# Optimization experiments

Hardware: AMD Instinct MI355X
Metric: run time of the kernel (lower is better)

Reference implementation:

```python
import jax, jax.numpy as jnp
import numpy as np

B, S, V, E, H, T = 128, 512, 6000, 100, 256, 9


def setup_inputs() -> dict:
    key = jax.random.key(0)
    ks = jax.random.split(key, 16)
    lengths = jax.random.randint(ks[0], (B,), S // 4, S + 1)
    mask = (jnp.arange(S)[None, :] < lengths[:, None])  # [B,S] bool, contiguous prefixes
    data = jax.random.randint(ks[1], (B, S), 1, V)
    data = jnp.where(mask, data, 0)  # pad token = 0 (padding_idx)
    sc = 0.1
    emb = jax.random.normal(ks[2], (V, E), jnp.float32) * sc
    emb = emb.at[0].set(0.0)  # padding_idx=0
    return {
        "data": data, "mask": mask,
        "emb": emb,
        "W_ih_f": jax.random.normal(ks[3], (4 * H, E), jnp.float32) * sc,
        "W_hh_f": jax.random.normal(ks[4], (4 * H, H), jnp.float32) * sc,
        "b_f": jax.random.normal(ks[5], (4 * H,), jnp.float32) * sc,
        "W_ih_b": jax.random.normal(ks[6], (4 * H, E), jnp.float32) * sc,
        "W_hh_b": jax.random.normal(ks[7], (4 * H, H), jnp.float32) * sc,
        "b_b": jax.random.normal(ks[8], (4 * H,), jnp.float32) * sc,
        "mlp_W": jax.random.normal(ks[9], (T, 2 * H), jnp.float32) * sc,
        "mlp_b": jax.random.normal(ks[10], (T,), jnp.float32) * sc,
        "start_trans": jax.random.normal(ks[11], (T,), jnp.float32) * sc,
        "trans": jax.random.normal(ks[12], (T, T), jnp.float32) * sc,
        "end_trans": jax.random.normal(ks[13], (T,), jnp.float32) * sc,
    }


def _lstm_dir(xg, W_hh, reverse):
    # xg: [S,B,4H] precomputed input projection + biases
    h0 = jnp.zeros((xg.shape[1], W_hh.shape[1]), xg.dtype)

    def step(carry, xt):
        h, c = carry
        g = xt + h @ W_hh.T
        i, f, gg, o = jnp.split(g, 4, axis=-1)  # PyTorch gate order i,f,g,o
        c = jax.nn.sigmoid(f) * c + jax.nn.sigmoid(i) * jnp.tanh(gg)
        h = jax.nn.sigmoid(o) * jnp.tanh(c)
        return (h, c), h

    _, hs = jax.lax.scan(step, (h0, h0), xg, reverse=reverse)
    return hs  # [S,B,H]


def _emissions(data, emb, W_ih_f, W_hh_f, b_f, W_ih_b, W_hh_b, b_b, mlp_W, mlp_b):
    x = emb[data]  # [B,S,E]
    xg_f = jnp.einsum('bse,ge->sbg', x, W_ih_f) + b_f
    xg_b = jnp.einsum('bse,ge->sbg', x, W_ih_b) + b_b
    hf = _lstm_dir(xg_f, W_hh_f, False)
    hb = _lstm_dir(xg_b, W_hh_b, True)
    h = jnp.concatenate([hf, hb], axis=-1)  # [S,B,2H]
    return jnp.einsum('sbh,th->bst', h, mlp_W) + mlp_b  # [B,S,T]


def _viterbi(em, mask, start_trans, trans, end_trans):
    b, s, t = em.shape
    score0 = start_trans + em[:, 0]  # [B,T]
    em_t = jnp.swapaxes(em, 0, 1)[1:]      # [S-1,B,T]
    mask_t = jnp.swapaxes(mask, 0, 1)[1:]  # [S-1,B]

    def step(score, inp):
        e_t, m_t = inp
        cand = score[:, :, None] + trans[None] + e_t[:, None, :]  # [B,Tprev,Tcur]
        new = cand.max(axis=1)
        bp = cand.argmax(axis=1).astype(jnp.int32)  # [B,T]
        score = jnp.where(m_t[:, None], new, score)
        return score, bp

    score, bps = jax.lax.scan(step, score0, (em_t, mask_t))
    final = score + end_trans
    best_score = final.max(axis=-1)               # [B]
    last_tag = final.argmax(axis=-1).astype(jnp.int32)

    def back(tag, inp):
        bp, m_t = inp
        prev = jnp.take_along_axis(bp, tag[:, None], axis=1)[:, 0]
        prev = jnp.where(m_t, prev, tag)
        return prev, tag

    first_tag, tags_rest = jax.lax.scan(back, last_tag, (bps, mask_t), reverse=True)
    paths = jnp.concatenate([first_tag[None], tags_rest], axis=0)  # [S,B]
    paths = jnp.where(jnp.swapaxes(mask, 0, 1), paths, 0)
    return jnp.swapaxes(paths, 0, 1), best_score


def reference(data, mask, emb, W_ih_f, W_hh_f, b_f, W_ih_b, W_hh_b, b_b,
              mlp_W, mlp_b, start_trans, trans, end_trans):
    em = _emissions(data, emb, W_ih_f, W_hh_f, b_f, W_ih_b, W_hh_b, b_b, mlp_W, mlp_b)
    paths, best_score = _viterbi(em, mask, start_trans, trans, end_trans)
    return paths, best_score
```

## Files before the change

### kernel.cpp

```cpp
#include <hip/hip_runtime.h>
#include <math.h>
#include <stdint.h>

#define B 128
#define S 512
#define V 6000
#define E 100
#define H 256
#define G4 1024
#define T 9

#define WREG 20
#define WLDS 3
#define WSTR 41

#define OFF_PEMB_F 0u
#define PEMB_BYTES (V*G4*4u)
#define OFF_PEMB_B (OFF_PEMB_F + PEMB_BYTES)
#define OFF_EMF    (OFF_PEMB_B + PEMB_BYTES)
#define EM_BYTES   (B*S*T*4u)
#define OFF_EMB    (OFF_EMF + EM_BYTES)
#define OFF_BP     (OFF_EMB + EM_BYTES)
#define BP_BYTES   ((S-1)*B*16u)
#define OFF_LT     (OFF_BP + BP_BYTES)
#define OFF_PT     (OFF_LT + 512u)
#define OFF_WSTREAM OFF_BP

__device__ __forceinline__ float sigf(float x) { return 1.0f / (1.0f + expf(-x)); }

__global__ __launch_bounds__(256) void k_pemb(const float* __restrict__ emb,
                                              const float* __restrict__ wf, const float* __restrict__ bf,
                                              const float* __restrict__ wb, const float* __restrict__ bb,
                                              char* __restrict__ ws) {
    int blk = blockIdx.x;
    int d   = blk >= 375;
    int vb  = d ? blk - 375 : blk;
    const float* W    = d ? wb : wf;
    const float* bias = d ? bb : bf;
    float* pe = (float*)(ws + (d ? OFF_PEMB_B : OFF_PEMB_F));

    __shared__ float es[16 * E];
    for (int i = threadIdx.x; i < 16 * E; i += 256) es[i] = emb[vb * 16 * E + i];
    __syncthreads();

    int j = threadIdx.x;
    float acc[4][16];
    #pragma unroll
    for (int q = 0; q < 4; q++) {
        float bq = bias[q * H + j];
        #pragma unroll
        for (int v = 0; v < 16; v++) acc[q][v] = bq;
    }
    for (int e = 0; e < E; e++) {
        float w0 = W[(0 * H + j) * E + e];
        float w1 = W[(1 * H + j) * E + e];
        float w2 = W[(2 * H + j) * E + e];
        float w3 = W[(3 * H + j) * E + e];
        #pragma unroll
        for (int v = 0; v < 16; v++) {
            float x = es[v * E + e];
            acc[0][v] += w0 * x; acc[1][v] += w1 * x;
            acc[2][v] += w2 * x; acc[3][v] += w3 * x;
        }
    }
    for (int v = 0; v < 16; v++)
        #pragma unroll
        for (int q = 0; q < 4; q++)
            pe[(vb * 16 + v) * G4 + q * H + j] = acc[q][v];
}

__global__ __launch_bounds__(256) void k_prep(const float* __restrict__ whhf,
                                              const float* __restrict__ whhb,
                                              char* __restrict__ ws) {
    int tid = blockIdx.x * 256 + threadIdx.x;
    if (tid >= 2 * WSTR * 1024) return;
    int d   = tid >= WSTR * 1024;
    int idx = d ? tid - WSTR * 1024 : tid;
    int g = idx >> 10, r = idx & 1023;
    const float* whh = d ? whhb : whhf;
    float4* wstr = (float4*)(ws + OFF_WSTREAM);
    const float4* src = (const float4*)(whh + (size_t)r * H + 4 * (WREG + WLDS));
    wstr[((size_t)(d * WSTR + g) << 10) + r] = src[g];
}

__global__ __attribute__((amdgpu_flat_work_group_size(512, 512), amdgpu_waves_per_eu(2, 2)))
void k_lstm(const int* __restrict__ data,
            const float* __restrict__ whhf,
            const float* __restrict__ whhb,
            const float* __restrict__ mlpW,
            char* __restrict__ ws) {
    int blk = blockIdx.x;
    int d = blk >> 7, b = blk & 127;
    const float* whh = d ? whhb : whhf;
    const float* pe  = (const float*)(ws + (d ? OFF_PEMB_B : OFF_PEMB_F));
    float* emdst = (float*)(ws + (d ? OFF_EMB : OFF_EMF));
    const float4* wstr = (const float4*)(ws + OFF_WSTREAM) + ((size_t)(d * WSTR) << 10);

    __shared__ __align__(16) float hs[H];
    __shared__ float4 sW[WLDS << 10];
    __shared__ float  gbuf[G4];
    __shared__ float  red[T][4];
    __shared__ int    toks[S];

    int t = threadIdx.x;
    int r0 = t, r1 = t + 512;

    const float4* wrow0 = (const float4*)(whh + (size_t)r0 * H);
    const float4* wrow1 = (const float4*)(whh + (size_t)r1 * H);
    float4 wA[WREG], wB[WREG];
    #pragma unroll
    for (int g = 0; g < WREG; g++) { wA[g] = wrow0[g]; wB[g] = wrow1[g]; }
    #pragma unroll
    for (int g = 0; g < WREG; g++) {
        asm volatile("" : "+v"(wA[g].x), "+v"(wA[g].y), "+v"(wA[g].z), "+v"(wA[g].w));
        asm volatile("" : "+v"(wB[g].x), "+v"(wB[g].y), "+v"(wB[g].z), "+v"(wB[g].w));
    }
    #pragma unroll
    for (int g = 0; g < WLDS; g++) {
        sW[(g << 10) + r0] = wrow0[WREG + g];
        sW[(g << 10) + r1] = wrow1[WREG + g];
    }

    toks[t] = data[b * S + t];

    float mw[T];
    if (t < 256) {
        #pragma unroll
        for (int tt = 0; tt < T; tt++) mw[tt] = mlpW[tt * (2 * H) + d * H + t];
    }
    if (t < H) hs[t] = 0.0f;
    float cst = 0.0f;
    __syncthreads();

    const float4* hs4 = (const float4*)hs;
    const float4* wsp0 = wstr + r0;
    const float4* wsp1 = wstr + r1;

    float pf0, pf1;
    {
        int sp0 = d ? (S - 1) : 0;
        size_t tok = (size_t)toks[sp0];
        pf0 = pe[(tok << 10) + r0];
        pf1 = pe[(tok << 10) + r1];
    }

    for (int ss = 0; ss < S; ss++) {
        int sp = d ? (S - 1 - ss) : ss;
        float acc0 = pf0, acc1 = pf1;
        if (ss + 1 < S) {
            int spn = d ? (S - 2 - ss) : (ss + 1);
            size_t tok = (size_t)toks[spn];
            pf0 = pe[(tok << 10) + r0];
            pf1 = pe[(tok << 10) + r1];
        }

        #pragma unroll
        for (int g = 0; g < WREG; g++) {
            float4 h4 = hs4[g];
            float4 a = wA[g], bb2 = wB[g];
            acc0 = fmaf(a.x, h4.x, acc0);  acc1 = fmaf(bb2.x, h4.x, acc1);
            acc0 = fmaf(a.y, h4.y, acc0);  acc1 = fmaf(bb2.y, h4.y, acc1);
            acc0 = fmaf(a.z, h4.z, acc0);  acc1 = fmaf(bb2.z, h4.z, acc1);
            acc0 = fmaf(a.w, h4.w, acc0);  acc1 = fmaf(bb2.w, h4.w, acc1);
        }
        #pragma unroll
        for (int g = 0; g < WLDS; g++) {
            float4 w0 = sW[(g << 10) + r0];
            float4 w1 = sW[(g << 10) + r1];
            float4 h4 = hs4[WREG + g];
            acc0 = fmaf(w0.x, h4.x, acc0);  acc1 = fmaf(w1.x, h4.x, acc1);
            acc0 = fmaf(w0.y, h4.y, acc0);  acc1 = fmaf(w1.y, h4.y, acc1);
            acc0 = fmaf(w0.z, h4.z, acc0);  acc1 = fmaf(w1.z, h4.z, acc1);
            acc0 = fmaf(w0.w, h4.w, acc0);  acc1 = fmaf(w1.w, h4.w, acc1);
        }
        #pragma unroll 4
        for (int g = 0; g < WSTR; g++) {
            float4 w0 = wsp0[(size_t)g << 10];
            float4 w1 = wsp1[(size_t)g << 10];
            float4 h4 = hs4[WREG + WLDS + g];
            acc0 = fmaf(w0.x, h4.x, acc0);  acc1 = fmaf(w1.x, h4.x, acc1);
            acc0 = fmaf(w0.y, h4.y, acc0);  acc1 = fmaf(w1.y, h4.y, acc1);
            acc0 = fmaf(w0.z, h4.z, acc0);  acc1 = fmaf(w1.z, h4.z, acc1);
            acc0 = fmaf(w0.w, h4.w, acc0);  acc1 = fmaf(w1.w, h4.w, acc1);
        }
        gbuf[r0] = acc0;
        gbuf[r1] = acc1;
        __syncthreads();

        if (t < 256) {
            float gi = gbuf[t], gf = gbuf[H + t], gg = gbuf[2 * H + t], go = gbuf[3 * H + t];
            float ig = sigf(gi), fg = sigf(gf), tg = tanhf(gg), og = sigf(go);
            cst = fg * cst + ig * tg;
            float hn = og * tanhf(cst);
            hs[t] = hn;
            int l = t & 63, wv = t >> 6;
            #pragma unroll
            for (int tt = 0; tt < T; tt++) {
                float v = hn * mw[tt];
                v += __shfl_xor(v, 32, 64); v += __shfl_xor(v, 16, 64);
                v += __shfl_xor(v, 8, 64);  v += __shfl_xor(v, 4, 64);
                v += __shfl_xor(v, 2, 64);  v += __shfl_xor(v, 1, 64);
                if (l == 0) red[tt][wv] = v;
            }
        }
        __syncthreads();
        if (t < T)
            emdst[((size_t)b * S + sp) * T + t] = red[t][0] + red[t][1] + red[t][2] + red[t][3];
    }
}

__global__ __launch_bounds__(64) void k_vit(const int* __restrict__ data,
                                            const float* __restrict__ strans,
                                            const float* __restrict__ trans,
                                            const float* __restrict__ etrans,
                                            const float* __restrict__ mlpb,
                                            float* __restrict__ out,
                                            char* __restrict__ ws) {
    int b = blockIdx.x, t = threadIdx.x;
    const float* emf = (const float*)(ws + OFF_EMF);
    const float* emb = (const float*)(ws + OFF_EMB);
    char* bp = ws + OFF_BP;
    int*  lt = (int*)(ws + OFF_LT);
    bool act = t < T;

    float trp[T];
    float mb = 0.0f;
    if (act) {
        #pragma unroll
        for (int p = 0; p < T; p++) trp[p] = trans[p * T + t];
        mb = mlpb[t];
    }
    float score = -1e30f;
    if (act) score = strans[t] + emf[(b * S) * T + t] + emb[(b * S) * T + t] + mb;

    for (int s = 1; s < S; s++) {
        float e = 0.0f;
        if (act) e = emf[(b * S + s) * T + t] + emb[(b * S + s) * T + t] + mb;
        float best = __shfl(score, 0, 64) + trp[0];
        int bpi = 0;
        #pragma unroll
        for (int p = 1; p < T; p++) {
            float cand = __shfl(score, p, 64) + trp[p];
            if (cand > best) { best = cand; bpi = p; }
        }
        int m = data[b * S + s] != 0;
        if (act) {
            score = m ? (best + e) : score;
            bp[((size_t)(s - 1) * B + b) * 16 + t] = (char)bpi;
        }
    }
    float fin = act ? score + etrans[t] : -1e30f;
    float bv = __shfl(fin, 0, 64);
    int bi = 0;
    #pragma unroll
    for (int p = 1; p < T; p++) {
        float v = __shfl(fin, p, 64);
        if (v > bv) { bv = v; bi = p; }
    }
    if (t == 0) { out[B * S + b] = bv; lt[b] = bi; }
}

__global__ __launch_bounds__(128) void k_back(const int* __restrict__ data, char* __restrict__ ws) {
    int b = threadIdx.x;
    const int4* bp4 = (const int4*)(ws + OFF_BP);
    const int*  lt  = (const int*)(ws + OFF_LT);
    int* pt = (int*)(ws + OFF_PT);
    int tag = lt[b];
    pt[(S - 1) * B + b] = tag;
    for (int p = S - 2; p >= 0; p--) {
        int4 r = bp4[(size_t)p * B + b];
        int m = data[b * S + p + 1] != 0;
        unsigned w = (unsigned)(tag < 8 ? (tag < 4 ? r.x : r.y) : r.z);
        int nt = (int)((w >> ((tag & 3) * 8)) & 0xff);
        tag = m ? nt : tag;
        pt[p * B + b] = tag;
    }
}

__global__ __launch_bounds__(256) void k_fin(const int* __restrict__ data,
                                             float* __restrict__ out,
                                             const char* __restrict__ ws) {
    int tid = blockIdx.x * 256 + threadIdx.x;
    const int* pt = (const int*)(ws + OFF_PT);
    int b = tid >> 9, p = tid & 511;
    out[tid] = (data[tid] != 0) ? (float)pt[p * B + b] : 0.0f;
}

extern "C" void kernel_launch(void* const* d_in, const int* in_sizes, int n_in,
                              void* d_out, int out_size, void* d_ws, size_t ws_size,
                              hipStream_t stream) {
    const int*   data = (const int*)d_in[0];
    const float* emb  = (const float*)d_in[2];
    const float* wihf = (const float*)d_in[3];
    const float* whhf = (const float*)d_in[4];
    const float* bf   = (const float*)d_in[5];
    const float* wihb = (const float*)d_in[6];
    const float* whhb = (const float*)d_in[7];
    const float* bb   = (const float*)d_in[8];
    const float* mlpW = (const float*)d_in[9];
    const float* mlpb = (const float*)d_in[10];
    const float* st   = (const float*)d_in[11];
    const float* tr   = (const float*)d_in[12];
    const float* et   = (const float*)d_in[13];
    float* out = (float*)d_out;
    char*  ws  = (char*)d_ws;

    hipLaunchKernelGGL(k_pemb, dim3(750),  dim3(256), 0, stream, emb, wihf, bf, wihb, bb, ws);
    hipLaunchKernelGGL(k_prep, dim3(328),  dim3(256), 0, stream, whhf, whhb, ws);
    hipLaunchKernelGGL(k_lstm, dim3(256),  dim3(512), 0, stream, data, whhf, whhb, mlpW, ws);
    hipLaunchKernelGGL(k_vit,  dim3(128),  dim3(64),  0, stream, data, st, tr, et, mlpb, out, ws);
    hipLaunchKernelGGL(k_back, dim3(1),    dim3(128), 0, stream, data, ws);
    hipLaunchKernelGGL(k_fin,  dim3(256),  dim3(256), 0, stream, data, out, ws);
}
```

Before: 4.772 ms.

## Process two batch rows per LSTM block with all four gates per thread

The recurrent LSTM kernel now handles two sequences per block with 256 threads, each computing all four gates of one hidden unit for both sequences. Each weight load is reused across two batch rows, and the gate-exchange shared buffer and one barrier per step are removed. h is double-buffered and the emission store is deferred by one step. The register-resident weight slice is dropped in favour of reading those columns from global/L2 each step, and the LDS weight share is increased. The trade-off is half as many blocks (128 instead of 256) and more global weight traffic per step.

```diff
diff --git a/kernel.cpp b/kernel.cpp
--- a/kernel.cpp
+++ b/kernel.cpp
@@ -10,8 +10,8 @@
 #define G4 1024
 #define T 9
 
-#define WREG 20
-#define WLDS 3
+#define WGLOB 15
+#define WLDS 8
 #define WSTR 41
 
 #define OFF_PEMB_F 0u
@@ -79,133 +79,209 @@
     int g = idx >> 10, r = idx & 1023;
     const float* whh = d ? whhb : whhf;
     float4* wstr = (float4*)(ws + OFF_WSTREAM);
-    const float4* src = (const float4*)(whh + (size_t)r * H + 4 * (WREG + WLDS));
+    const float4* src = (const float4*)(whh + (size_t)r * H + 4 * (WGLOB + WLDS));
     wstr[((size_t)(d * WSTR + g) << 10) + r] = src[g];
 }
 
-__global__ __attribute__((amdgpu_flat_work_group_size(512, 512), amdgpu_waves_per_eu(2, 2)))
+__global__ __attribute__((amdgpu_flat_work_group_size(256, 256), amdgpu_waves_per_eu(1, 1)))
 void k_lstm(const int* __restrict__ data,
             const float* __restrict__ whhf,
             const float* __restrict__ whhb,
             const float* __restrict__ mlpW,
             char* __restrict__ ws) {
     int blk = blockIdx.x;
-    int d = blk >> 7, b = blk & 127;
+    int d = blk >> 6, p = blk & 63;
+    int b0 = 2 * p, b1 = b0 + 1;
     const float* whh = d ? whhb : whhf;
     const float* pe  = (const float*)(ws + (d ? OFF_PEMB_B : OFF_PEMB_F));
     float* emdst = (float*)(ws + (d ? OFF_EMB : OFF_EMF));
     const float4* wstr = (const float4*)(ws + OFF_WSTREAM) + ((size_t)(d * WSTR) << 10);
 
-    __shared__ __align__(16) float hs[H];
+    __shared__ __align__(16) float hs[2][2][H];
     __shared__ float4 sW[WLDS << 10];
-    __shared__ float  gbuf[G4];
-    __shared__ float  red[T][4];
-    __shared__ int    toks[S];
+    __shared__ float  red[2][2][T][4];
+    __shared__ int    toks[2][S];
 
     int t = threadIdx.x;
-    int r0 = t, r1 = t + 512;
-
-    const float4* wrow0 = (const float4*)(whh + (size_t)r0 * H);
-    const float4* wrow1 = (const float4*)(whh + (size_t)r1 * H);
-    float4 wA[WREG], wB[WREG];
-    #pragma unroll
-    for (int g = 0; g < WREG; g++) { wA[g] = wrow0[g]; wB[g] = wrow1[g]; }
-    #pragma unroll
-    for (int g = 0; g < WREG; g++) {
-        asm volatile("" : "+v"(wA[g].x), "+v"(wA[g].y), "+v"(wA[g].z), "+v"(wA[g].w));
-        asm volatile("" : "+v"(wB[g].x), "+v"(wB[g].y), "+v"(wB[g].z), "+v"(wB[g].w));
-    }
+
+    const float4* wr0 = (const float4*)(whh + (size_t)(t        ) * H);
+    const float4* wr1 = (const float4*)(whh + (size_t)(t +  256 ) * H);
+    const float4* wr2 = (const float4*)(whh + (size_t)(t +  512 ) * H);
+    const float4* wr3 = (const float4*)(whh + (size_t)(t +  768 ) * H);
+
     #pragma unroll
     for (int g = 0; g < WLDS; g++) {
-        sW[(g << 10) + r0] = wrow0[WREG + g];
-        sW[(g << 10) + r1] = wrow1[WREG + g];
-    }
-
-    toks[t] = data[b * S + t];
+        sW[(g << 10) + t       ] = wr0[WGLOB + g];
+        sW[(g << 10) + t +  256] = wr1[WGLOB + g];
+        sW[(g << 10) + t +  512] = wr2[WGLOB + g];
+        sW[(g << 10) + t +  768] = wr3[WGLOB + g];
+    }
+
+    toks[0][t]       = data[b0 * S + t];
+    toks[0][t + 256] = data[b0 * S + t + 256];
+    toks[1][t]       = data[b1 * S + t];
+    toks[1][t + 256] = data[b1 * S + t + 256];
 
     float mw[T];
-    if (t < 256) {
-        #pragma unroll
-        for (int tt = 0; tt < T; tt++) mw[tt] = mlpW[tt * (2 * H) + d * H + t];
-    }
-    if (t < H) hs[t] = 0.0f;
-    float cst = 0.0f;
+    #pragma unroll
+    for (int tt = 0; tt < T; tt++) mw[tt] = mlpW[tt * (2 * H) + d * H + t];
+
+    hs[0][0][t] = 0.0f;
+    hs[0][1][t] = 0.0f;
+    float c0 = 0.0f, c1 = 0.0f;
     __syncthreads();
 
-    const float4* hs4 = (const float4*)hs;
-    const float4* wsp0 = wstr + r0;
-    const float4* wsp1 = wstr + r1;
-
-    float pf0, pf1;
+    const float4* wsp = wstr + t;
+
+    float pf[4][2];
     {
         int sp0 = d ? (S - 1) : 0;
-        size_t tok = (size_t)toks[sp0];
-        pf0 = pe[(tok << 10) + r0];
-        pf1 = pe[(tok << 10) + r1];
-    }
-
+        size_t tk0 = (size_t)toks[0][sp0];
+        size_t tk1 = (size_t)toks[1][sp0];
+        #pragma unroll
+        for (int k = 0; k < 4; k++) {
+            pf[k][0] = pe[(tk0 << 10) + t + (k << 8)];
+            pf[k][1] = pe[(tk1 << 10) + t + (k << 8)];
+        }
+    }
+
+    int spPrev = 0;
     for (int ss = 0; ss < S; ss++) {
         int sp = d ? (S - 1 - ss) : ss;
-        float acc0 = pf0, acc1 = pf1;
+        int par = ss & 1;
+
+        if (ss > 0 && t < T) {
+            int pp = par ^ 1;
+            emdst[((size_t)b0 * S + spPrev) * T + t] =
+                red[pp][0][t][0] + red[pp][0][t][1] + red[pp][0][t][2] + red[pp][0][t][3];
+            emdst[((size_t)b1 * S + spPrev) * T + t] =
+                red[pp][1][t][0] + red[pp][1][t][1] + red[pp][1][t][2] + red[pp][1][t][3];
+        }
+
+        float acc[4][2];
+        #pragma unroll
+        for (int k = 0; k < 4; k++) { acc[k][0] = pf[k][0]; acc[k][1] = pf[k][1]; }
+
         if (ss + 1 < S) {
             int spn = d ? (S - 2 - ss) : (ss + 1);
-            size_t tok = (size_t)toks[spn];
-            pf0 = pe[(tok << 10) + r0];
-            pf1 = pe[(tok << 10) + r1];
-        }
-
-        #pragma unroll
-        for (int g = 0; g < WREG; g++) {
-            float4 h4 = hs4[g];
-            float4 a = wA[g], bb2 = wB[g];
-            acc0 = fmaf(a.x, h4.x, acc0);  acc1 = fmaf(bb2.x, h4.x, acc1);
-            acc0 = fmaf(a.y, h4.y, acc0);  acc1 = fmaf(bb2.y, h4.y, acc1);
-            acc0 = fmaf(a.z, h4.z, acc0);  acc1 = fmaf(bb2.z, h4.z, acc1);
-            acc0 = fmaf(a.w, h4.w, acc0);  acc1 = fmaf(bb2.w, h4.w, acc1);
+            size_t tk0 = (size_t)toks[0][spn];
+            size_t tk1 = (size_t)toks[1][spn];
+            #pragma unroll
+            for (int k = 0; k < 4; k++) {
+                pf[k][0] = pe[(tk0 << 10) + t + (k << 8)];
+                pf[k][1] = pe[(tk1 << 10) + t + (k << 8)];
+            }
+        }
+
+        const float4* h0p = (const float4*)&hs[par][0][0];
+        const float4* h1p = (const float4*)&hs[par][1][0];
+
+        #pragma unroll 5
+        for (int g = 0; g < WGLOB; g++) {
+            float4 h0 = h0p[g], h1 = h1p[g];
+            float4 w0 = wr0[g], w1 = wr1[g], w2 = wr2[g], w3 = wr3[g];
+            acc[0][0] = fmaf(w0.x, h0.x, acc[0][0]);  acc[0][1] = fmaf(w0.x, h1.x, acc[0][1]);
+            acc[1][0] = fmaf(w1.x, h0.x, acc[1][0]);  acc[1][1] = fmaf(w1.x, h1.x, acc[1][1]);
+            acc[2][0] = fmaf(w2.x, h0.x, acc[2][0]);  acc[2][1] = fmaf(w2.x, h1.x, acc[2][1]);
+            acc[3][0] = fmaf(w3.x, h0.x, acc[3][0]);  acc[3][1] = fmaf(w3.x, h1.x, acc[3][1]);
+            acc[0][0] = fmaf(w0.y, h0.y, acc[0][0]);  acc[0][1] = fmaf(w0.y, h1.y, acc[0][1]);
+            acc[1][0] = fmaf(w1.y, h0.y, acc[1][0]);  acc[1][1] = fmaf(w1.y, h1.y, acc[1][1]);
+            acc[2][0] = fmaf(w2.y, h0.y, acc[2][0]);  acc[2][1] = fmaf(w2.y, h1.y, acc[2][1]);
+            acc[3][0] = fmaf(w3.y, h0.y, acc[3][0]);  acc[3][1] = fmaf(w3.y, h1.y, acc[3][1]);
+            acc[0][0] = fmaf(w0.z, h0.z, acc[0][0]);  acc[0][1] = fmaf(w0.z, h1.z, acc[0][1]);
+            acc[1][0] = fmaf(w1.z, h0.z, acc[1][0]);  acc[1][1] = fmaf(w1.z, h1.z, acc[1][1]);
+            acc[2][0] = fmaf(w2.z, h0.z, acc[2][0]);  acc[2][1] = fmaf(w2.z, h1.z, acc[2][1]);
+            acc[3][0] = fmaf(w3.z, h0.z, acc[3][0]);  acc[3][1] = fmaf(w3.z, h1.z, acc[3][1]);
+            acc[0][0] = fmaf(w0.w, h0.w, acc[0][0]);  acc[0][1] = fmaf(w0.w, h1.w, acc[0][1]);
+            acc[1][0] = fmaf(w1.w, h0.w, acc[1][0]);  acc[1][1] = fmaf(w1.w, h1.w, acc[1][1]);
+            acc[2][0] = fmaf(w2.w, h0.w, acc[2][0]);  acc[2][1] = fmaf(w2.w, h1.w, acc[2][1]);
+            acc[3][0] = fmaf(w3.w, h0.w, acc[3][0]);  acc[3][1] = fmaf(w3.w, h1.w, acc[3][1]);
         }
         #pragma unroll
         for (int g = 0; g < WLDS; g++) {
-            float4 w0 = sW[(g << 10) + r0];
-            float4 w1 = sW[(g << 10) + r1];
-            float4 h4 = hs4[WREG + g];
-            acc0 = fmaf(w0.x, h4.x, acc0);  acc1 = fmaf(w1.x, h4.x, acc1);
-            acc0 = fmaf(w0.y, h4.y, acc0);  acc1 = fmaf(w1.y, h4.y, acc1);
-            acc0 = fmaf(w0.z, h4.z, acc0);  acc1 = fmaf(w1.z, h4.z, acc1);
-            acc0 = fmaf(w0.w, h4.w, acc0);  acc1 = fmaf(w1.w, h4.w, acc1);
-        }
-        #pragma unroll 4
+            float4 h0 = h0p[WGLOB + g], h1 = h1p[WGLOB + g];
+            float4 w0 = sW[(g << 10) + t       ];
+            float4 w1 = sW[(g << 10) + t +  256];
+            float4 w2 = sW[(g << 10) + t +  512];
+            float4 w3 = sW[(g << 10) + t +  768];
+            acc[0][0] = fmaf(w0.x, h0.x, acc[0][0]);  acc[0][1] = fmaf(w0.x, h1.x, acc[0][1]);
+            acc[1][0] = fmaf(w1.x, h0.x, acc[1][0]);  acc[1][1] = fmaf(w1.x, h1.x, acc[1][1]);
+            acc[2][0] = fmaf(w2.x, h0.x, acc[2][0]);  acc[2][1] = fmaf(w2.x, h1.x, acc[2][1]);
+            acc[3][0] = fmaf(w3.x, h0.x, acc[3][0]);  acc[3][1] = fmaf(w3.x, h1.x, acc[3][1]);
+            acc[0][0] = fmaf(w0.y, h0.y, acc[0][0]);  acc[0][1] = fmaf(w0.y, h1.y, acc[0][1]);
+            acc[1][0] = fmaf(w1.y, h0.y, acc[1][0]);  acc[1][1] = fmaf(w1.y, h1.y, acc[1][1]);
+            acc[2][0] = fmaf(w2.y, h0.y, acc[2][0]);  acc[2][1] = fmaf(w2.y, h1.y, acc[2][1]);
+            acc[3][0] = fmaf(w3.y, h0.y, acc[3][0]);  acc[3][1] = fmaf(w3.y, h1.y, acc[3][1]);
+            acc[0][0] = fmaf(w0.z, h0.z, acc[0][0]);  acc[0][1] = fmaf(w0.z, h1.z, acc[0][1]);
+            acc[1][0] = fmaf(w1.z, h0.z, acc[1][0]);  acc[1][1] = fmaf(w1.z, h1.z, acc[1][1]);
+            acc[2][0] = fmaf(w2.z, h0.z, acc[2][0]);  acc[2][1] = fmaf(w2.z, h1.z, acc[2][1]);
+            acc[3][0] = fmaf(w3.z, h0.z, acc[3][0]);  acc[3][1] = fmaf(w3.z, h1.z, acc[3][1]);
+            acc[0][0] = fmaf(w0.w, h0.w, acc[0][0]);  acc[0][1] = fmaf(w0.w, h1.w, acc[0][1]);
+            acc[1][0] = fmaf(w1.w, h0.w, acc[1][0]);  acc[1][1] = fmaf(w1.w, h1.w, acc[1][1]);
+            acc[2][0] = fmaf(w2.w, h0.w, acc[2][0]);  acc[2][1] = fmaf(w2.w, h1.w, acc[2][1]);
+            acc[3][0] = fmaf(w3.w, h0.w, acc[3][0]);  acc[3][1] = fmaf(w3.w, h1.w, acc[3][1]);
+        }
+        #pragma unroll 8
         for (int g = 0; g < WSTR; g++) {
-            float4 w0 = wsp0[(size_t)g << 10];
-            float4 w1 = wsp1[(size_t)g << 10];
-            float4 h4 = hs4[WREG + WLDS + g];
-            acc0 = fmaf(w0.x, h4.x, acc0);  acc1 = fmaf(w1.x, h4.x, acc1);
-            acc0 = fmaf(w0.y, h4.y, acc0);  acc1 = fmaf(w1.y, h4.y, acc1);
-            acc0 = fmaf(w0.z, h4.z, acc0);  acc1 = fmaf(w1.z, h4.z, acc1);
-            acc0 = fmaf(w0.w, h4.w, acc0);  acc1 = fmaf(w1.w, h4.w, acc1);
-        }
-        gbuf[r0] = acc0;
-        gbuf[r1] = acc1;
+            float4 h0 = h0p[WGLOB + WLDS + g], h1 = h1p[WGLOB + WLDS + g];
+            const float4* wg = wsp + ((size_t)g << 10);
+            float4 w0 = wg[0], w1 = wg[256], w2 = wg[512], w3 = wg[768];
+            acc[0][0] = fmaf(w0.x, h0.x, acc[0][0]);  acc[0][1] = fmaf(w0.x, h1.x, acc[0][1]);
+            acc[1][0] = fmaf(w1.x, h0.x, acc[1][0]);  acc[1][1] = fmaf(w1.x, h1.x, acc[1][1]);
+            acc[2][0] = fmaf(w2.x, h0.x, acc[2][0]);  acc[2][1] = fmaf(w2.x, h1.x, acc[2][1]);
+            acc[3][0] = fmaf(w3.x, h0.x, acc[3][0]);  acc[3][1] = fmaf(w3.x, h1.x, acc[3][1]);
+            acc[0][0] = fmaf(w0.y, h0.y, acc[0][0]);  acc[0][1] = fmaf(w0.y, h1.y, acc[0][1]);
+            acc[1][0] = fmaf(w1.y, h0.y, acc[1][0]);  acc[1][1] = fmaf(w1.y, h1.y, acc[1][1]);
+            acc[2][0] = fmaf(w2.y, h0.y, acc[2][0]);  acc[2][1] = fmaf(w2.y, h1.y, acc[2][1]);
+            acc[3][0] = fmaf(w3.y, h0.y, acc[3][0]);  acc[3][1] = fmaf(w3.y, h1.y, acc[3][1]);
+            acc[0][0] = fmaf(w0.z, h0.z, acc[0][0]);  acc[0][1] = fmaf(w0.z, h1.z, acc[0][1]);
+            acc[1][0] = fmaf(w1.z, h0.z, acc[1][0]);  acc[1][1] = fmaf(w1.z, h1.z, acc[1][1]);
+            acc[2][0] = fmaf(w2.z, h0.z, acc[2][0]);  acc[2][1] = fmaf(w2.z, h1.z, acc[2][1]);
+            acc[3][0] = fmaf(w3.z, h0.z, acc[3][0]);  acc[3][1] = fmaf(w3.z, h1.z, acc[3][1]);
+            acc[0][0] = fmaf(w0.w, h0.w, acc[0][0]);  acc[0][1] = fmaf(w0.w, h1.w, acc[0][1]);
+            acc[1][0] = fmaf(w1.w, h0.w, acc[1][0]);  acc[1][1] = fmaf(w1.w, h1.w, acc[1][1]);
+            acc[2][0] = fmaf(w2.w, h0.w, acc[2][0]);  acc[2][1] = fmaf(w2.w, h1.w, acc[2][1]);
+            acc[3][0] = fmaf(w3.w, h0.w, acc[3][0]);  acc[3][1] = fmaf(w3.w, h1.w, acc[3][1]);
+        }
+
+        int nxt = par ^ 1;
+        float hn0, hn1;
+        {
+            float ig = sigf(acc[0][0]), fg = sigf(acc[1][0]);
+            float tg = tanhf(acc[2][0]), og = sigf(acc[3][0]);
+            c0 = fg * c0 + ig * tg;
+            hn0 = og * tanhf(c0);
+            hs[nxt][0][t] = hn0;
+        }
+        {
+            float ig = sigf(acc[0][1]), fg = sigf(acc[1][1]);
+            float tg = tanhf(acc[2][1]), og = sigf(acc[3][1]);
+            c1 = fg * c1 + ig * tg;
+            hn1 = og * tanhf(c1);
+            hs[nxt][1][t] = hn1;
+        }
+        int l = t & 63, wv = t >> 6;
+        #pragma unroll
+        for (int tt = 0; tt < T; tt++) {
+            float v0 = hn0 * mw[tt];
+            float v1 = hn1 * mw[tt];
+            v0 += __shfl_xor(v0, 32, 64);  v1 += __shfl_xor(v1, 32, 64);
+            v0 += __shfl_xor(v0, 16, 64);  v1 += __shfl_xor(v1, 16, 64);
+            v0 += __shfl_xor(v0, 8, 64);   v1 += __shfl_xor(v1, 8, 64);
+            v0 += __shfl_xor(v0, 4, 64);   v1 += __shfl_xor(v1, 4, 64);
+            v0 += __shfl_xor(v0, 2, 64);   v1 += __shfl_xor(v1, 2, 64);
+            v0 += __shfl_xor(v0, 1, 64);   v1 += __shfl_xor(v1, 1, 64);
+            if (l == 0) { red[par][0][tt][wv] = v0; red[par][1][tt][wv] = v1; }
+        }
+        spPrev = sp;
         __syncthreads();
-
-        if (t < 256) {
-            float gi = gbuf[t], gf = gbuf[H + t], gg = gbuf[2 * H + t], go = gbuf[3 * H + t];
-            float ig = sigf(gi), fg = sigf(gf), tg = tanhf(gg), og = sigf(go);
-            cst = fg * cst + ig * tg;
-            float hn = og * tanhf(cst);
-            hs[t] = hn;
-            int l = t & 63, wv = t >> 6;
-            #pragma unroll
-            for (int tt = 0; tt < T; tt++) {
-                float v = hn * mw[tt];
-                v += __shfl_xor(v, 32, 64); v += __shfl_xor(v, 16, 64);
-                v += __shfl_xor(v, 8, 64);  v += __shfl_xor(v, 4, 64);
-                v += __shfl_xor(v, 2, 64);  v += __shfl_xor(v, 1, 64);
-                if (l == 0) red[tt][wv] = v;
-            }
-        }
-        __syncthreads();
-        if (t < T)
-            emdst[((size_t)b * S + sp) * T + t] = red[t][0] + red[t][1] + red[t][2] + red[t][3];
+    }
+    if (t < T) {
+        int pp = (S - 1) & 1;
+        emdst[((size_t)b0 * S + spPrev) * T + t] =
+            red[pp][0][t][0] + red[pp][0][t][1] + red[pp][0][t][2] + red[pp][0][t][3];
+        emdst[((size_t)b1 * S + spPrev) * T + t] =
+            red[pp][1][t][0] + red[pp][1][t][1] + red[pp][1][t][2] + red[pp][1][t][3];
     }
 }
 
@@ -307,7 +383,7 @@
 
     hipLaunchKernelGGL(k_pemb, dim3(750),  dim3(256), 0, stream, emb, wihf, bf, wihb, bb, ws);
     hipLaunchKernelGGL(k_prep, dim3(328),  dim3(256), 0, stream, whhf, whhb, ws);
-    hipLaunchKernelGGL(k_lstm, dim3(256),  dim3(512), 0, stream, data, whhf, whhb, mlpW, ws);
+    hipLaunchKernelGGL(k_lstm, dim3(128),  dim3(256), 0, stream, data, whhf, whhb, mlpW, ws);
     hipLaunchKernelGGL(k_vit,  dim3(128),  dim3(64),  0, stream, data, st, tr, et, mlpb, out, ws);
     hipLaunchKernelGGL(k_back, dim3(1),    dim3(128), 0, stream, data, ws);
     hipLaunchKernelGGL(k_fin,  dim3(256),  dim3(256), 0, stream, data, out, ws);
```

New measurement: 8.474 ms. 77.6% more time.

## Split hidden-dim reduction across thread halves with four gate rows per thread

Applied to the files above, without the earlier changes.

Each thread now owns all four gate rows of one hidden unit and covers one half of the hidden-state reduction dimension. The first half uses register, LDS and L2-streamed weights; the second half streams only. Partial sums are exchanged through a float4 LDS buffer, so the gate nonlinearities read contiguous i/f/g/o values. The aim is to rebalance the per-step matvec, but it moves ten register chunks per row to per-step global reloads. That raises total weight traffic each step and leaves the second half fully memory-bound.

```diff
diff --git a/kernel.cpp b/kernel.cpp
--- a/kernel.cpp
+++ b/kernel.cpp
@@ -98,27 +98,34 @@
 
     __shared__ __align__(16) float hs[H];
     __shared__ float4 sW[WLDS << 10];
-    __shared__ float  gbuf[G4];
+    __shared__ __align__(16) float4 pbuf[2][256];
     __shared__ float  red[T][4];
     __shared__ int    toks[S];
 
     int t = threadIdx.x;
-    int r0 = t, r1 = t + 512;
-
-    const float4* wrow0 = (const float4*)(whh + (size_t)r0 * H);
-    const float4* wrow1 = (const float4*)(whh + (size_t)r1 * H);
-    float4 wA[WREG], wB[WREG];
+    int u = t & 255, half = t >> 8;
+
+    const float4* wr0 = (const float4*)(whh + (size_t)(u      ) * H);
+    const float4* wr1 = (const float4*)(whh + (size_t)(u + 256) * H);
+    const float4* wr2 = (const float4*)(whh + (size_t)(u + 512) * H);
+    const float4* wr3 = (const float4*)(whh + (size_t)(u + 768) * H);
+
+    float4 wPa[10], wPb[10], wPc[10], wPd[10];
     #pragma unroll
-    for (int g = 0; g < WREG; g++) { wA[g] = wrow0[g]; wB[g] = wrow1[g]; }
+    for (int g = 0; g < 10; g++) {
+        wPa[g] = wr0[g]; wPb[g] = wr1[g]; wPc[g] = wr2[g]; wPd[g] = wr3[g];
+    }
     #pragma unroll
-    for (int g = 0; g < WREG; g++) {
-        asm volatile("" : "+v"(wA[g].x), "+v"(wA[g].y), "+v"(wA[g].z), "+v"(wA[g].w));
-        asm volatile("" : "+v"(wB[g].x), "+v"(wB[g].y), "+v"(wB[g].z), "+v"(wB[g].w));
-    }
-    #pragma unroll
-    for (int g = 0; g < WLDS; g++) {
-        sW[(g << 10) + r0] = wrow0[WREG + g];
-        sW[(g << 10) + r1] = wrow1[WREG + g];
+    for (int g = 0; g < 10; g++) {
+        asm volatile("" : "+v"(wPa[g].x), "+v"(wPa[g].y), "+v"(wPa[g].z), "+v"(wPa[g].w));
+        asm volatile("" : "+v"(wPb[g].x), "+v"(wPb[g].y), "+v"(wPb[g].z), "+v"(wPb[g].w));
+        asm volatile("" : "+v"(wPc[g].x), "+v"(wPc[g].y), "+v"(wPc[g].z), "+v"(wPc[g].w));
+        asm volatile("" : "+v"(wPd[g].x), "+v"(wPd[g].y), "+v"(wPd[g].z), "+v"(wPd[g].w));
+    }
+
+    for (int i = t; i < (WLDS << 10); i += 512) {
+        int g = i >> 10, r = i & 1023;
+        sW[i] = ((const float4*)(whh + (size_t)r * H))[WREG + g];
     }
 
     toks[t] = data[b * S + t];
@@ -133,63 +140,112 @@
     __syncthreads();
 
     const float4* hs4 = (const float4*)hs;
-    const float4* wsp0 = wstr + r0;
-    const float4* wsp1 = wstr + r1;
-
-    float pf0, pf1;
-    {
+
+    float pf0 = 0.0f, pf1 = 0.0f, pf2 = 0.0f, pf3 = 0.0f;
+    if (half == 0) {
         int sp0 = d ? (S - 1) : 0;
         size_t tok = (size_t)toks[sp0];
-        pf0 = pe[(tok << 10) + r0];
-        pf1 = pe[(tok << 10) + r1];
+        pf0 = pe[(tok << 10) + u];
+        pf1 = pe[(tok << 10) + u + 256];
+        pf2 = pe[(tok << 10) + u + 512];
+        pf3 = pe[(tok << 10) + u + 768];
     }
 
     for (int ss = 0; ss < S; ss++) {
         int sp = d ? (S - 1 - ss) : ss;
-        float acc0 = pf0, acc1 = pf1;
-        if (ss + 1 < S) {
+        float a0, a1, a2, a3;
+        if (half == 0) { a0 = pf0; a1 = pf1; a2 = pf2; a3 = pf3; }
+        else           { a0 = a1 = a2 = a3 = 0.0f; }
+
+        if (half == 0 && ss + 1 < S) {
             int spn = d ? (S - 2 - ss) : (ss + 1);
             size_t tok = (size_t)toks[spn];
-            pf0 = pe[(tok << 10) + r0];
-            pf1 = pe[(tok << 10) + r1];
-        }
-
-        #pragma unroll
-        for (int g = 0; g < WREG; g++) {
-            float4 h4 = hs4[g];
-            float4 a = wA[g], bb2 = wB[g];
-            acc0 = fmaf(a.x, h4.x, acc0);  acc1 = fmaf(bb2.x, h4.x, acc1);
-            acc0 = fmaf(a.y, h4.y, acc0);  acc1 = fmaf(bb2.y, h4.y, acc1);
-            acc0 = fmaf(a.z, h4.z, acc0);  acc1 = fmaf(bb2.z, h4.z, acc1);
-            acc0 = fmaf(a.w, h4.w, acc0);  acc1 = fmaf(bb2.w, h4.w, acc1);
-        }
-        #pragma unroll
-        for (int g = 0; g < WLDS; g++) {
-            float4 w0 = sW[(g << 10) + r0];
-            float4 w1 = sW[(g << 10) + r1];
-            float4 h4 = hs4[WREG + g];
-            acc0 = fmaf(w0.x, h4.x, acc0);  acc1 = fmaf(w1.x, h4.x, acc1);
-            acc0 = fmaf(w0.y, h4.y, acc0);  acc1 = fmaf(w1.y, h4.y, acc1);
-            acc0 = fmaf(w0.z, h4.z, acc0);  acc1 = fmaf(w1.z, h4.z, acc1);
-            acc0 = fmaf(w0.w, h4.w, acc0);  acc1 = fmaf(w1.w, h4.w, acc1);
-        }
-        #pragma unroll 4
-        for (int g = 0; g < WSTR; g++) {
-            float4 w0 = wsp0[(size_t)g << 10];
-            float4 w1 = wsp1[(size_t)g << 10];
-            float4 h4 = hs4[WREG + WLDS + g];
-            acc0 = fmaf(w0.x, h4.x, acc0);  acc1 = fmaf(w1.x, h4.x, acc1);
-            acc0 = fmaf(w0.y, h4.y, acc0);  acc1 = fmaf(w1.y, h4.y, acc1);
-            acc0 = fmaf(w0.z, h4.z, acc0);  acc1 = fmaf(w1.z, h4.z, acc1);
-            acc0 = fmaf(w0.w, h4.w, acc0);  acc1 = fmaf(w1.w, h4.w, acc1);
-        }
-        gbuf[r0] = acc0;
-        gbuf[r1] = acc1;
+            pf0 = pe[(tok << 10) + u];
+            pf1 = pe[(tok << 10) + u + 256];
+            pf2 = pe[(tok << 10) + u + 512];
+            pf3 = pe[(tok << 10) + u + 768];
+        }
+
+        if (half == 0) {
+            #pragma unroll
+            for (int g = 0; g < 10; g++) {
+                float4 h4 = hs4[g];
+                a0 = fmaf(wPa[g].x, h4.x, a0);  a1 = fmaf(wPb[g].x, h4.x, a1);
+                a2 = fmaf(wPc[g].x, h4.x, a2);  a3 = fmaf(wPd[g].x, h4.x, a3);
+                a0 = fmaf(wPa[g].y, h4.y, a0);  a1 = fmaf(wPb[g].y, h4.y, a1);
+                a2 = fmaf(wPc[g].y, h4.y, a2);  a3 = fmaf(wPd[g].y, h4.y, a3);
+                a0 = fmaf(wPa[g].z, h4.z, a0);  a1 = fmaf(wPb[g].z, h4.z, a1);
+                a2 = fmaf(wPc[g].z, h4.z, a2);  a3 = fmaf(wPd[g].z, h4.z, a3);
+                a0 = fmaf(wPa[g].w, h4.w, a0);  a1 = fmaf(wPb[g].w, h4.w, a1);
+                a2 = fmaf(wPc[g].w, h4.w, a2);  a3 = fmaf(wPd[g].w, h4.w, a3);
+            }
+            #pragma unroll
+            for (int g = 10; g < WREG; g++) {
+                float4 h4 = hs4[g];
+                float4 w0 = wr0[g], w1 = wr1[g], w2 = wr2[g], w3 = wr3[g];
+                a0 = fmaf(w0.x, h4.x, a0);  a1 = fmaf(w1.x, h4.x, a1);
+                a2 = fmaf(w2.x, h4.x, a2);  a3 = fmaf(w3.x, h4.x, a3);
+                a0 = fmaf(w0.y, h4.y, a0);  a1 = fmaf(w1.y, h4.y, a1);
+                a2 = fmaf(w2.y, h4.y, a2);  a3 = fmaf(w3.y, h4.y, a3);
+                a0 = fmaf(w0.z, h4.z, a0);  a1 = fmaf(w1.z, h4.z, a1);
+                a2 = fmaf(w2.z, h4.z, a2);  a3 = fmaf(w3.z, h4.z, a3);
+                a0 = fmaf(w0.w, h4.w, a0);  a1 = fmaf(w1.w, h4.w, a1);
+                a2 = fmaf(w2.w, h4.w, a2);  a3 = fmaf(w3.w, h4.w, a3);
+            }
+            #pragma unroll
+            for (int g = 0; g < WLDS; g++) {
+                float4 h4 = hs4[WREG + g];
+                float4 w0 = sW[(g << 10) + u      ];
+                float4 w1 = sW[(g << 10) + u + 256];
+                float4 w2 = sW[(g << 10) + u + 512];
+                float4 w3 = sW[(g << 10) + u + 768];
+                a0 = fmaf(w0.x, h4.x, a0);  a1 = fmaf(w1.x, h4.x, a1);
+                a2 = fmaf(w2.x, h4.x, a2);  a3 = fmaf(w3.x, h4.x, a3);
+                a0 = fmaf(w0.y, h4.y, a0);  a1 = fmaf(w1.y, h4.y, a1);
+                a2 = fmaf(w2.y, h4.y, a2);  a3 = fmaf(w3.y, h4.y, a3);
+                a0 = fmaf(w0.z, h4.z, a0);  a1 = fmaf(w1.z, h4.z, a1);
+                a2 = fmaf(w2.z, h4.z, a2);  a3 = fmaf(w3.z, h4.z, a3);
+                a0 = fmaf(w0.w, h4.w, a0);  a1 = fmaf(w1.w, h4.w, a1);
+                a2 = fmaf(w2.w, h4.w, a2);  a3 = fmaf(w3.w, h4.w, a3);
+            }
+            #pragma unroll 3
+            for (int g = 0; g < 9; g++) {
+                float4 h4 = hs4[WREG + WLDS + g];
+                const float4* wg = wstr + ((size_t)g << 10) + u;
+                float4 w0 = wg[0], w1 = wg[256], w2 = wg[512], w3 = wg[768];
+                a0 = fmaf(w0.x, h4.x, a0);  a1 = fmaf(w1.x, h4.x, a1);
+                a2 = fmaf(w2.x, h4.x, a2);  a3 = fmaf(w3.x, h4.x, a3);
+                a0 = fmaf(w0.y, h4.y, a0);  a1 = fmaf(w1.y, h4.y, a1);
+                a2 = fmaf(w2.y, h4.y, a2);  a3 = fmaf(w3.y, h4.y, a3);
+                a0 = fmaf(w0.z, h4.z, a0);  a1 = fmaf(w1.z, h4.z, a1);
+                a2 = fmaf(w2.z, h4.z, a2);  a3 = fmaf(w3.z, h4.z, a3);
+                a0 = fmaf(w0.w, h4.w, a0);  a1 = fmaf(w1.w, h4.w, a1);
+                a2 = fmaf(w2.w, h4.w, a2);  a3 = fmaf(w3.w, h4.w, a3);
+            }
+        } else {
+            #pragma unroll 4
+            for (int g = 0; g < 32; g++) {
+                float4 h4 = hs4[32 + g];
+                const float4* wg = wstr + ((size_t)(9 + g) << 10) + u;
+                float4 w0 = wg[0], w1 = wg[256], w2 = wg[512], w3 = wg[768];
+                a0 = fmaf(w0.x, h4.x, a0);  a1 = fmaf(w1.x, h4.x, a1);
+                a2 = fmaf(w2.x, h4.x, a2);  a3 = fmaf(w3.x, h4.x, a3);
+                a0 = fmaf(w0.y, h4.y, a0);  a1 = fmaf(w1.y, h4.y, a1);
+                a2 = fmaf(w2.y, h4.y, a2);  a3 = fmaf(w3.y, h4.y, a3);
+                a0 = fmaf(w0.z, h4.z, a0);  a1 = fmaf(w1.z, h4.z, a1);
+                a2 = fmaf(w2.z, h4.z, a2);  a3 = fmaf(w3.z, h4.z, a3);
+                a0 = fmaf(w0.w, h4.w, a0);  a1 = fmaf(w1.w, h4.w, a1);
+                a2 = fmaf(w2.w, h4.w, a2);  a3 = fmaf(w3.w, h4.w, a3);
+            }
+        }
+
+        pbuf[half][u] = make_float4(a0, a1, a2, a3);
         __syncthreads();
 
         if (t < 256) {
-            float gi = gbuf[t], gf = gbuf[H + t], gg = gbuf[2 * H + t], go = gbuf[3 * H + t];
-            float ig = sigf(gi), fg = sigf(gf), tg = tanhf(gg), og = sigf(go);
+            float4 pa = pbuf[0][t], pb = pbuf[1][t];
+            float ig = sigf(pa.x + pb.x), fg = sigf(pa.y + pb.y);
+            float tg = tanhf(pa.z + pb.z), og = sigf(pa.w + pb.w);
             cst = fg * cst + ig * tg;
             float hn = og * tanhf(cst);
             hs[t] = hn;
```

Result: slower. 10.44 ms (+118.7%).
